# Optimization experiments

Measured on AMD Instinct MI355X. Metric: run time of the kernel, lower is better.

Reference implementation:

```python
import jax, jax.numpy as jnp
import numpy as np

D_MODEL = 1024
NUM_HEADS = 16
D_FF = 4096
NEG_INF = -1e9


def _linear_params(key, d_in, d_out):
    kw, kb = jax.random.split(key)
    bound = 1.0 / np.sqrt(d_in)
    W = jax.random.uniform(kw, (d_in, d_out), jnp.float32, -bound, bound)
    b = jax.random.uniform(kb, (d_out,), jnp.float32, -bound, bound)
    return W, b


def setup_inputs() -> dict:
    key = jax.random.key(0)
    ks = jax.random.split(key, 8)
    B, S = 2, 2048
    x = jax.random.normal(ks[0], (B, S, D_MODEL), jnp.float32)
    # causal mask: 1 = attend, 0 = masked
    mask = jnp.tril(jnp.ones((S, S), jnp.bool_))[None, :, :]
    Wq, bq = _linear_params(ks[1], D_MODEL, D_MODEL)
    Wk, bk = _linear_params(ks[2], D_MODEL, D_MODEL)
    Wv, bv = _linear_params(ks[3], D_MODEL, D_MODEL)
    Wo, bo = _linear_params(ks[4], D_MODEL, D_MODEL)
    W1, b1 = _linear_params(ks[5], D_MODEL, D_FF)
    W2, b2 = _linear_params(ks[6], D_FF, D_MODEL)
    ln1_g = jnp.ones((D_MODEL,), jnp.float32)
    ln1_b = jnp.zeros((D_MODEL,), jnp.float32)
    ln2_g = jnp.ones((D_MODEL,), jnp.float32)
    ln2_b = jnp.zeros((D_MODEL,), jnp.float32)
    return {"x": x, "mask": mask,
            "Wq": Wq, "bq": bq, "Wk": Wk, "bk": bk, "Wv": Wv, "bv": bv,
            "Wo": Wo, "bo": bo, "W1": W1, "b1": b1, "W2": W2, "b2": b2,
            "ln1_g": ln1_g, "ln1_b": ln1_b, "ln2_g": ln2_g, "ln2_b": ln2_b}


def layer_norm(x, g, b, eps=1e-5):
    mu = jnp.mean(x, axis=-1, keepdims=True)
    var = jnp.mean(jnp.square(x - mu), axis=-1, keepdims=True)
    return (x - mu) * jax.lax.rsqrt(var + eps) * g + b


def attention(xn, mask, Wq, bq, Wk, bk, Wv, bv, Wo, bo):
    B, S, D = xn.shape
    H, dk = NUM_HEADS, D // NUM_HEADS
    q = (xn @ Wq + bq).reshape(B, S, H, dk).transpose(0, 2, 1, 3)  # [B,H,S,dk]
    k = (xn @ Wk + bk).reshape(B, S, H, dk).transpose(0, 2, 1, 3)
    v = (xn @ Wv + bv).reshape(B, S, H, dk).transpose(0, 2, 1, 3)
    scores = jnp.einsum("bhsd,bhtd->bhst", q, k) / jnp.sqrt(jnp.float32(dk))
    scores = jnp.where(mask[:, None, :, :], scores, NEG_INF)
    attn = jax.nn.softmax(scores, axis=-1)
    out = jnp.einsum("bhst,bhtd->bhsd", attn, v)  # [B,H,S,dk]
    out = out.transpose(0, 2, 1, 3).reshape(B, S, D)
    return out @ Wo + bo


def reference(x, mask, Wq, bq, Wk, bk, Wv, bv, Wo, bo, W1, b1, W2, b2,
              ln1_g, ln1_b, ln2_g, ln2_b):
    # pre-norm MHA + residual (dropout = identity at eval)
    h = x + attention(layer_norm(x, ln1_g, ln1_b), mask,
                      Wq, bq, Wk, bk, Wv, bv, Wo, bo)
    # pre-norm FFN + residual
    ff = jax.nn.relu(layer_norm(h, ln2_g, ln2_b) @ W1 + b1) @ W2 + b2
    return h + ff
```

## Files before the change

### kernel.cpp

```cpp
#include <hip/hip_runtime.h>

typedef unsigned short u16;
typedef __attribute__((ext_vector_type(8))) short    s16x8;
typedef __attribute__((ext_vector_type(8))) unsigned short u16x8;
typedef __attribute__((ext_vector_type(4))) float    f32x4;

typedef __attribute__((address_space(1))) const void gvoid_c;
typedef __attribute__((address_space(3))) void       lvoid;

__device__ __forceinline__ float b2f(u16 x) {
    return __builtin_bit_cast(float, (unsigned)x << 16);
}
__device__ __forceinline__ u16 f2bf(float f) {
    unsigned u = __builtin_bit_cast(unsigned, f);
    return (u16)((u + 0x7FFFu + ((u >> 16) & 1u)) >> 16);
}
__device__ __forceinline__ void gld16(const void* g, void* l) {
    __builtin_amdgcn_global_load_lds((gvoid_c*)g, (lvoid*)l, 16, 0, 0);
}

__global__ __launch_bounds__(256) void transpose_f2b(
    const float* __restrict__ in, u16* __restrict__ out, int R, int C)
{
    __shared__ u16 tile[32][33];
    int tx = threadIdx.x & 31, ty = threadIdx.x >> 5;
    int c0 = blockIdx.x * 32, r0 = blockIdx.y * 32;
#pragma unroll
    for (int i = 0; i < 32; i += 8)
        tile[ty + i][tx] = f2bf(in[(size_t)(r0 + ty + i) * C + c0 + tx]);
    __syncthreads();
#pragma unroll
    for (int i = 0; i < 32; i += 8)
        out[(size_t)(c0 + ty + i) * R + r0 + tx] = tile[tx][ty + i];
}

__global__ void concat3(const float* a, const float* b, const float* c, float* o) {
    int i = blockIdx.x * blockDim.x + threadIdx.x;
    o[i] = (i < 1024) ? a[i] : (i < 2048 ? b[i - 1024] : c[i - 2048]);
}

__global__ __launch_bounds__(256) void ln_k(
    const float* __restrict__ in, const float* __restrict__ gg,
    const float* __restrict__ bb, u16* __restrict__ out)
{
    const int D = 1024;
    int row  = blockIdx.x * 4 + (threadIdx.x >> 6);
    int lane = threadIdx.x & 63;
    const float* ip = in + (size_t)row * D;
    float v[16];
#pragma unroll
    for (int cc = 0; cc < 4; cc++) {
        f32x4 t = *(const f32x4*)(ip + cc * 256 + lane * 4);
#pragma unroll
        for (int i = 0; i < 4; i++) v[cc * 4 + i] = t[i];
    }
    float s1 = 0.f, s2 = 0.f;
#pragma unroll
    for (int i = 0; i < 16; i++) { s1 += v[i]; s2 += v[i] * v[i]; }
#pragma unroll
    for (int m = 1; m < 64; m <<= 1) { s1 += __shfl_xor(s1, m); s2 += __shfl_xor(s2, m); }
    float mu   = s1 * (1.f / 1024.f);
    float var  = s2 * (1.f / 1024.f) - mu * mu;
    float rstd = rsqrtf(var + 1e-5f);
#pragma unroll
    for (int cc = 0; cc < 4; cc++) {
        int e = cc * 256 + lane * 4;
        f32x4 gv = *(const f32x4*)(gg + e);
        f32x4 bv = *(const f32x4*)(bb + e);
        u16 o[4];
#pragma unroll
        for (int i = 0; i < 4; i++)
            o[i] = f2bf((v[cc * 4 + i] - mu) * rstd * gv[i] + bv[i]);
        *(__attribute__((ext_vector_type(4))) unsigned short*)(out + (size_t)row * D + e) =
            (__attribute__((ext_vector_type(4))) unsigned short){o[0], o[1], o[2], o[3]};
    }
}

template <int RES, bool RELU, bool OUTF32>
__global__ __launch_bounds__(256) void gemm_bt(
    const u16* __restrict__ A, const u16* __restrict__ Bt,
    const float* __restrict__ bias, const float* __restrict__ res,
    void* __restrict__ out, int M, int N, int K)
{
    __shared__ u16 As[4096];
    __shared__ u16 Bs[4096];
    int tid = threadIdx.x, wave = tid >> 6, lane = tid & 63;
    int g = lane >> 4, c = lane & 15;
    int wm = wave >> 1, wn = wave & 1;
    int m0 = blockIdx.y * 128, n0 = blockIdx.x * 128;

    f32x4 acc[4][4];
#pragma unroll
    for (int m = 0; m < 4; m++)
#pragma unroll
        for (int n = 0; n < 4; n++) acc[m][n] = (f32x4){0, 0, 0, 0};

    int ch0 = wave * 128 + lane, ch1 = ch0 + 64;
    const u16* Ag0 = A  + (size_t)(m0 + (ch0 >> 2)) * K + (ch0 & 3) * 8;
    const u16* Ag1 = A  + (size_t)(m0 + (ch1 >> 2)) * K + (ch1 & 3) * 8;
    const u16* Bg0 = Bt + (size_t)(n0 + (ch0 >> 2)) * K + (ch0 & 3) * 8;
    const u16* Bg1 = Bt + (size_t)(n0 + (ch1 >> 2)) * K + (ch1 & 3) * 8;
    u16* Al0 = &As[wave * 1024];
    u16* Al1 = &As[wave * 1024 + 512];
    u16* Bl0 = &Bs[wave * 1024];
    u16* Bl1 = &Bs[wave * 1024 + 512];

    for (int k0 = 0; k0 < K; k0 += 32) {
        __syncthreads();
        gld16(Ag0, Al0); gld16(Ag1, Al1);
        gld16(Bg0, Bl0); gld16(Bg1, Bl1);
        Ag0 += 32; Ag1 += 32; Bg0 += 32; Bg1 += 32;
        __syncthreads();
        s16x8 af[4], bfr[4];
#pragma unroll
        for (int m = 0; m < 4; m++)
            af[m] = *(const s16x8*)&As[(wm * 64 + m * 16 + c) * 32 + g * 8];
#pragma unroll
        for (int n = 0; n < 4; n++)
            bfr[n] = *(const s16x8*)&Bs[(wn * 64 + n * 16 + c) * 32 + g * 8];
#pragma unroll
        for (int m = 0; m < 4; m++)
#pragma unroll
            for (int n = 0; n < 4; n++)
                acc[m][n] = __builtin_amdgcn_mfma_f32_16x16x32_bf16(af[m], bfr[n], acc[m][n], 0, 0, 0);
    }

#pragma unroll
    for (int n = 0; n < 4; n++) {
        int col = n0 + wn * 64 + n * 16 + c;
        float bb = bias[col];
#pragma unroll
        for (int m = 0; m < 4; m++) {
#pragma unroll
            for (int j = 0; j < 4; j++) {
                int row = m0 + wm * 64 + m * 16 + g * 4 + j;
                float v = acc[m][n][j] + bb;
                if (RES == 2) v += res[(size_t)row * N + col];
                if (RELU) v = fmaxf(v, 0.f);
                if (OUTF32) ((float*)out)[(size_t)row * N + col] = v;
                else        ((u16*)out)[(size_t)row * N + col] = f2bf(v);
            }
        }
    }
}

template <int RES, bool RELU, bool OUTF32>
__global__ __launch_bounds__(256) void gemm_bt_n64(
    const u16* __restrict__ A, const u16* __restrict__ Bt,
    const float* __restrict__ bias, const float* __restrict__ res,
    void* __restrict__ out, int M, int N, int K)
{
    __shared__ u16 As[4096];
    __shared__ u16 Bs[2048];
    int tid = threadIdx.x, wave = tid >> 6, lane = tid & 63;
    int g = lane >> 4, c = lane & 15;
    int wm = wave >> 1, wn = wave & 1;
    int m0 = blockIdx.y * 128, n0 = blockIdx.x * 64;

    f32x4 acc[4][2];
#pragma unroll
    for (int m = 0; m < 4; m++)
#pragma unroll
        for (int n = 0; n < 2; n++) acc[m][n] = (f32x4){0, 0, 0, 0};

    int ch0 = wave * 128 + lane, ch1 = ch0 + 64;
    int chb = wave * 64 + lane;
    const u16* Ag0 = A  + (size_t)(m0 + (ch0 >> 2)) * K + (ch0 & 3) * 8;
    const u16* Ag1 = A  + (size_t)(m0 + (ch1 >> 2)) * K + (ch1 & 3) * 8;
    const u16* Bg0 = Bt + (size_t)(n0 + (chb >> 2)) * K + (chb & 3) * 8;
    u16* Al0 = &As[wave * 1024];
    u16* Al1 = &As[wave * 1024 + 512];
    u16* Bl0 = &Bs[wave * 512];

    for (int k0 = 0; k0 < K; k0 += 32) {
        __syncthreads();
        gld16(Ag0, Al0); gld16(Ag1, Al1);
        gld16(Bg0, Bl0);
        Ag0 += 32; Ag1 += 32; Bg0 += 32;
        __syncthreads();
        s16x8 af[4], bfr[2];
#pragma unroll
        for (int m = 0; m < 4; m++)
            af[m] = *(const s16x8*)&As[(wm * 64 + m * 16 + c) * 32 + g * 8];
#pragma unroll
        for (int n = 0; n < 2; n++)
            bfr[n] = *(const s16x8*)&Bs[(wn * 32 + n * 16 + c) * 32 + g * 8];
#pragma unroll
        for (int m = 0; m < 4; m++)
#pragma unroll
            for (int n = 0; n < 2; n++)
                acc[m][n] = __builtin_amdgcn_mfma_f32_16x16x32_bf16(af[m], bfr[n], acc[m][n], 0, 0, 0);
    }

#pragma unroll
    for (int n = 0; n < 2; n++) {
        int col = n0 + wn * 32 + n * 16 + c;
        float bb = bias[col];
#pragma unroll
        for (int m = 0; m < 4; m++) {
#pragma unroll
            for (int j = 0; j < 4; j++) {
                int row = m0 + wm * 64 + m * 16 + g * 4 + j;
                float v = acc[m][n][j] + bb;
                if (RES == 2) v += res[(size_t)row * N + col];
                if (RELU) v = fmaxf(v, 0.f);
                if (OUTF32) ((float*)out)[(size_t)row * N + col] = v;
                else        ((u16*)out)[(size_t)row * N + col] = f2bf(v);
            }
        }
    }
}

__global__ __launch_bounds__(256) void v_transpose(
    const u16* __restrict__ qkv, u16* __restrict__ vt)
{
    const int S = 2048, NC = 3072;
    __shared__ u16 tile[64][72];
    int st = blockIdx.x, bh = blockIdx.y, b = bh >> 4, h = bh & 15;
    int tid = threadIdx.x;
    int i = tid >> 3, cb8 = (tid & 7) * 8;
    const u16* src = qkv + (size_t)(b * S + st * 64) * NC + 2048 + h * 64;
    u16x8 a0 = *(const u16x8*)(src + (size_t)i * NC + cb8);
    u16x8 a1 = *(const u16x8*)(src + (size_t)(i + 32) * NC + cb8);
    *(u16x8*)&tile[i][cb8]      = a0;
    *(u16x8*)&tile[i + 32][cb8] = a1;
    __syncthreads();
    int d = tid >> 3, e8 = (tid & 7) * 8;
    int m = (d & 7) * 8;
#pragma unroll
    for (int rr = 0; rr < 2; rr++) {
        int r = d + rr * 32;
        u16x8 o;
#pragma unroll
        for (int j = 0; j < 8; j++) o[j] = tile[(e8 ^ m) + j][r];
        *(u16x8*)(vt + ((size_t)bh * 64 + r) * 2048 + st * 64 + e8) = o;
    }
}

__global__ __launch_bounds__(256) void attn_fwd2(
    const u16* __restrict__ qkv, const u16* __restrict__ vt,
    u16* __restrict__ o)
{
    const int S = 2048, NC = 3072;
    __shared__ u16 Ks[4096];
    __shared__ u16 Vs[4096];
    __shared__ u16 Plds[4][16][72];
    int qp = blockIdx.x, bh = blockIdx.y, b = bh >> 4, h = bh & 15;
    int tid = threadIdx.x, wave = tid >> 6, lane = tid & 63;
    int g = lane >> 4, c = lane & 15;
    int sr = tid >> 3, scb8 = (tid & 7) * 8;
    int mS = (sr & 7) * 8;
    int mR = (c & 7) * 8;

    const u16* kbase = qkv + (size_t)b * S * NC + 1024 + h * 64;
    const u16* vbase = vt + (size_t)bh * 64 * 2048;

#pragma unroll 1
    for (int ph = 0; ph < 2; ph++) {
        int qt = ph ? qp : 31 - qp;
        int q0 = qt * 64 + wave * 16;
        const u16* qptr = qkv + (size_t)(b * S + q0 + c) * NC + h * 64;
        s16x8 qf0 = *(const s16x8*)(qptr + g * 8);
        s16x8 qf1 = *(const s16x8*)(qptr + 32 + g * 8);

        float mr[4], lr[4];
        f32x4 acc[4];
#pragma unroll
        for (int j = 0; j < 4; j++) { mr[j] = -1e30f; lr[j] = 0.f; }
#pragma unroll
        for (int n = 0; n < 4; n++) acc[n] = (f32x4){0, 0, 0, 0};

        int ntiles = qt + 1;
        for (int t = 0; t < ntiles; t++) {
            int t0 = t * 64;
            __syncthreads();
            gld16(kbase + (size_t)(t0 + sr)      * NC + (scb8 ^ mS), &Ks[wave * 512]);
            gld16(kbase + (size_t)(t0 + sr + 32) * NC + (scb8 ^ mS), &Ks[2048 + wave * 512]);
            gld16(vbase + (size_t)sr        * 2048 + t0 + scb8, &Vs[wave * 512]);
            gld16(vbase + (size_t)(sr + 32) * 2048 + t0 + scb8, &Vs[2048 + wave * 512]);
            __syncthreads();

            f32x4 s[4];
#pragma unroll
            for (int kt = 0; kt < 4; kt++) {
                int r = kt * 16 + c;
                s16x8 kf0 = *(const s16x8*)&Ks[r * 64 + ((g * 8) ^ mR)];
                s16x8 kf1 = *(const s16x8*)&Ks[r * 64 + ((32 + g * 8) ^ mR)];
                f32x4 sv = (f32x4){0, 0, 0, 0};
                sv = __builtin_amdgcn_mfma_f32_16x16x32_bf16(qf0, kf0, sv, 0, 0, 0);
                sv = __builtin_amdgcn_mfma_f32_16x16x32_bf16(qf1, kf1, sv, 0, 0, 0);
                s[kt] = sv;
            }
#pragma unroll
            for (int kt = 0; kt < 4; kt++) {
                int kcol = t0 + kt * 16 + c;
#pragma unroll
                for (int j = 0; j < 4; j++) {
                    int qrow = q0 + g * 4 + j;
                    s[kt][j] = (kcol <= qrow) ? s[kt][j] * 0.125f : -1e30f;
                }
            }
#pragma unroll
            for (int j = 0; j < 4; j++) {
                float tm = fmaxf(fmaxf(s[0][j], s[1][j]), fmaxf(s[2][j], s[3][j]));
#pragma unroll
                for (int m = 1; m < 16; m <<= 1) tm = fmaxf(tm, __shfl_xor(tm, m));
                float mnew = fmaxf(mr[j], tm);
                float corr = __expf(mr[j] - mnew);
                float rs = 0.f;
#pragma unroll
                for (int kt = 0; kt < 4; kt++) { float p = __expf(s[kt][j] - mnew); s[kt][j] = p; rs += p; }
#pragma unroll
                for (int m = 1; m < 16; m <<= 1) rs += __shfl_xor(rs, m);
                lr[j] = lr[j] * corr + rs;
                mr[j] = mnew;
#pragma unroll
                for (int n = 0; n < 4; n++) acc[n][j] *= corr;
            }
#pragma unroll
            for (int kt = 0; kt < 4; kt++)
#pragma unroll
                for (int j = 0; j < 4; j++)
                    Plds[wave][g * 4 + j][kt * 16 + c] = f2bf(s[kt][j]);
            s16x8 pa0 = *(const s16x8*)&Plds[wave][c][g * 8];
            s16x8 pa1 = *(const s16x8*)&Plds[wave][c][32 + g * 8];
#pragma unroll
            for (int n = 0; n < 4; n++) {
                int r = n * 16 + c;
                s16x8 vb0 = *(const s16x8*)&Vs[r * 64 + ((g * 8) ^ mR)];
                s16x8 vb1 = *(const s16x8*)&Vs[r * 64 + ((32 + g * 8) ^ mR)];
                acc[n] = __builtin_amdgcn_mfma_f32_16x16x32_bf16(pa0, vb0, acc[n], 0, 0, 0);
                acc[n] = __builtin_amdgcn_mfma_f32_16x16x32_bf16(pa1, vb1, acc[n], 0, 0, 0);
            }
        }
#pragma unroll
        for (int j = 0; j < 4; j++) {
            float inv = 1.f / lr[j];
            size_t rbase = (size_t)(b * S + q0 + g * 4 + j) * 1024 + h * 64;
#pragma unroll
            for (int n = 0; n < 4; n++)
                o[rbase + n * 16 + c] = f2bf(acc[n][j] * inv);
        }
    }
}

extern "C" void kernel_launch(void* const* d_in, const int* in_sizes, int n_in,
                              void* d_out, int out_size, void* d_ws, size_t ws_size,
                              hipStream_t stream)
{
    const float* x    = (const float*)d_in[0];
    const float* Wq   = (const float*)d_in[2];  const float* bq = (const float*)d_in[3];
    const float* Wk   = (const float*)d_in[4];  const float* bk = (const float*)d_in[5];
    const float* Wv   = (const float*)d_in[6];  const float* bv = (const float*)d_in[7];
    const float* Wo   = (const float*)d_in[8];  const float* bo = (const float*)d_in[9];
    const float* W1   = (const float*)d_in[10]; const float* b1 = (const float*)d_in[11];
    const float* W2   = (const float*)d_in[12]; const float* b2 = (const float*)d_in[13];
    const float* ln1g = (const float*)d_in[14]; const float* ln1b = (const float*)d_in[15];
    const float* ln2g = (const float*)d_in[16]; const float* ln2b = (const float*)d_in[17];

    unsigned char* ws = (unsigned char*)d_ws;
    u16*   Wqkv_t = (u16*)(ws + 0);
    u16*   Wo_t   = (u16*)(ws + 6291456);
    u16*   W1_t   = (u16*)(ws + 8388608);
    u16*   W2_t   = (u16*)(ws + 16777216);
    float* bqkv   = (float*)(ws + 25165824);
    u16*   lnbuf  = (u16*)(ws + 25178112);
    u16*   qkvbuf = (u16*)(ws + 33566720);
    u16*   attnb  = (u16*)(ws + 58732544);
    u16*   f1buf  = (u16*)(ws + 33566720);
    float* hbuf   = (float*)(ws + 67121152);
    u16*   vtbuf  = (u16*)(ws + 67121152);

    transpose_f2b<<<dim3(32, 32), 256, 0, stream>>>(Wq, Wqkv_t,               1024, 1024);
    transpose_f2b<<<dim3(32, 32), 256, 0, stream>>>(Wk, Wqkv_t + 1024 * 1024, 1024, 1024);
    transpose_f2b<<<dim3(32, 32), 256, 0, stream>>>(Wv, Wqkv_t + 2048 * 1024, 1024, 1024);
    transpose_f2b<<<dim3(32, 32), 256, 0, stream>>>(Wo, Wo_t,                 1024, 1024);
    transpose_f2b<<<dim3(128, 32), 256, 0, stream>>>(W1, W1_t,                1024, 4096);
    transpose_f2b<<<dim3(32, 128), 256, 0, stream>>>(W2, W2_t,                4096, 1024);
    concat3<<<12, 256, 0, stream>>>(bq, bk, bv, bqkv);

    ln_k<<<1024, 256, 0, stream>>>(x, ln1g, ln1b, lnbuf);
    gemm_bt<0, false, false><<<dim3(24, 32), 256, 0, stream>>>(
        lnbuf, Wqkv_t, bqkv, nullptr, qkvbuf, 4096, 3072, 1024);
    v_transpose<<<dim3(32, 32), 256, 0, stream>>>(qkvbuf, vtbuf);
    attn_fwd2<<<dim3(16, 32), 256, 0, stream>>>(qkvbuf, vtbuf, attnb);

    gemm_bt_n64<2, false, true><<<dim3(16, 32), 256, 0, stream>>>(
        attnb, Wo_t, bo, x, hbuf, 4096, 1024, 1024);

    ln_k<<<1024, 256, 0, stream>>>(hbuf, ln2g, ln2b, lnbuf);
    gemm_bt<0, true, false><<<dim3(32, 32), 256, 0, stream>>>(
        lnbuf, W1_t, b1, nullptr, f1buf, 4096, 4096, 1024);
    gemm_bt_n64<2, false, true><<<dim3(16, 32), 256, 0, stream>>>(
        f1buf, W2_t, b2, hbuf, (float*)d_out, 4096, 1024, 4096);
}
```

Baseline: 431.4 us.

## Double-buffer GEMM LDS staging and split-K the FFN2 GEMM with atomics

Merges the two GEMM kernels into one templated kernel that double-buffers the LDS tiles, so the next K-slice's global-to-LDS load is issued while the current slice runs MFMAs, and one barrier per iteration is dropped. The FFN down-projection (K=4096) now uses 128-wide tiles with a 4-way split-K over blockIdx.z. A separate init kernel writes residual plus bias into the output first, and the partial sums are then accumulated with relaxed fp32 atomics. This aims to hide load latency and improve occupancy for the long-K GEMM, at the cost of doubled LDS per block, atomic traffic, and summation order that can vary from run to run.

After: 445.3 us. 1.03x slower.

```diff
diff --git a/kernel.cpp b/kernel.cpp
--- a/kernel.cpp
+++ b/kernel.cpp
@@ -76,136 +76,103 @@
     }
 }
 
-template <int RES, bool RELU, bool OUTF32>
-__global__ __launch_bounds__(256) void gemm_bt(
+__global__ __launch_bounds__(256) void ffn2_init(
+    const float* __restrict__ h, const float* __restrict__ b2,
+    float* __restrict__ out)
+{
+    int i = blockIdx.x * 256 + threadIdx.x;
+    f32x4 hv = ((const f32x4*)h)[i];
+    f32x4 bv = ((const f32x4*)b2)[i & 255];
+    ((f32x4*)out)[i] = hv + bv;
+}
+
+template <int BN, int RES, bool RELU, bool OUTF32, bool ATOMIC>
+__global__ __launch_bounds__(256) void gemm2(
     const u16* __restrict__ A, const u16* __restrict__ Bt,
     const float* __restrict__ bias, const float* __restrict__ res,
-    void* __restrict__ out, int M, int N, int K)
-{
-    __shared__ u16 As[4096];
-    __shared__ u16 Bs[4096];
+    void* __restrict__ out, int M, int N, int K, int KC)
+{
+    constexpr int NFR = BN / 32;
+    __shared__ u16 As[2][4096];
+    __shared__ u16 Bs[2][BN * 32];
     int tid = threadIdx.x, wave = tid >> 6, lane = tid & 63;
     int g = lane >> 4, c = lane & 15;
     int wm = wave >> 1, wn = wave & 1;
-    int m0 = blockIdx.y * 128, n0 = blockIdx.x * 128;
-
-    f32x4 acc[4][4];
+    int m0 = blockIdx.y * 128, n0 = blockIdx.x * BN;
+    int kst = blockIdx.z * KC;
+
+    f32x4 acc[4][NFR];
 #pragma unroll
     for (int m = 0; m < 4; m++)
 #pragma unroll
-        for (int n = 0; n < 4; n++) acc[m][n] = (f32x4){0, 0, 0, 0};
+        for (int n = 0; n < NFR; n++) acc[m][n] = (f32x4){0, 0, 0, 0};
 
     int ch0 = wave * 128 + lane, ch1 = ch0 + 64;
-    const u16* Ag0 = A  + (size_t)(m0 + (ch0 >> 2)) * K + (ch0 & 3) * 8;
-    const u16* Ag1 = A  + (size_t)(m0 + (ch1 >> 2)) * K + (ch1 & 3) * 8;
-    const u16* Bg0 = Bt + (size_t)(n0 + (ch0 >> 2)) * K + (ch0 & 3) * 8;
-    const u16* Bg1 = Bt + (size_t)(n0 + (ch1 >> 2)) * K + (ch1 & 3) * 8;
-    u16* Al0 = &As[wave * 1024];
-    u16* Al1 = &As[wave * 1024 + 512];
-    u16* Bl0 = &Bs[wave * 1024];
-    u16* Bl1 = &Bs[wave * 1024 + 512];
-
-    for (int k0 = 0; k0 < K; k0 += 32) {
+    const u16* Ag0 = A + (size_t)(m0 + (ch0 >> 2)) * K + kst + (ch0 & 3) * 8;
+    const u16* Ag1 = A + (size_t)(m0 + (ch1 >> 2)) * K + kst + (ch1 & 3) * 8;
+    const u16* Bg0;
+    const u16* Bg1 = nullptr;
+    if constexpr (BN == 128) {
+        Bg0 = Bt + (size_t)(n0 + (ch0 >> 2)) * K + kst + (ch0 & 3) * 8;
+        Bg1 = Bt + (size_t)(n0 + (ch1 >> 2)) * K + kst + (ch1 & 3) * 8;
+    } else {
+        int chb = wave * 64 + lane;
+        Bg0 = Bt + (size_t)(n0 + (chb >> 2)) * K + kst + (chb & 3) * 8;
+    }
+
+    auto stage = [&](int buf, int kk) {
+        gld16(Ag0 + kk, &As[buf][wave * 1024]);
+        gld16(Ag1 + kk, &As[buf][wave * 1024 + 512]);
+        if constexpr (BN == 128) {
+            gld16(Bg0 + kk, &Bs[buf][wave * 1024]);
+            gld16(Bg1 + kk, &Bs[buf][wave * 1024 + 512]);
+        } else {
+            gld16(Bg0 + kk, &Bs[buf][wave * 512]);
+        }
+    };
+
+    int nt = KC / 32;
+    stage(0, 0);
+    __syncthreads();
+    int cur = 0;
+    for (int t = 0; t < nt; t++) {
+        if (t + 1 < nt) stage(cur ^ 1, (t + 1) * 32);
+        s16x8 af[4], bfr[NFR];
+#pragma unroll
+        for (int m = 0; m < 4; m++)
+            af[m] = *(const s16x8*)&As[cur][(wm * 64 + m * 16 + c) * 32 + g * 8];
+#pragma unroll
+        for (int n = 0; n < NFR; n++)
+            bfr[n] = *(const s16x8*)&Bs[cur][(wn * (BN / 2) + n * 16 + c) * 32 + g * 8];
+#pragma unroll
+        for (int m = 0; m < 4; m++)
+#pragma unroll
+            for (int n = 0; n < NFR; n++)
+                acc[m][n] = __builtin_amdgcn_mfma_f32_16x16x32_bf16(af[m], bfr[n], acc[m][n], 0, 0, 0);
         __syncthreads();
-        gld16(Ag0, Al0); gld16(Ag1, Al1);
-        gld16(Bg0, Bl0); gld16(Bg1, Bl1);
-        Ag0 += 32; Ag1 += 32; Bg0 += 32; Bg1 += 32;
-        __syncthreads();
-        s16x8 af[4], bfr[4];
-#pragma unroll
-        for (int m = 0; m < 4; m++)
-            af[m] = *(const s16x8*)&As[(wm * 64 + m * 16 + c) * 32 + g * 8];
-#pragma unroll
-        for (int n = 0; n < 4; n++)
-            bfr[n] = *(const s16x8*)&Bs[(wn * 64 + n * 16 + c) * 32 + g * 8];
-#pragma unroll
-        for (int m = 0; m < 4; m++)
-#pragma unroll
-            for (int n = 0; n < 4; n++)
-                acc[m][n] = __builtin_amdgcn_mfma_f32_16x16x32_bf16(af[m], bfr[n], acc[m][n], 0, 0, 0);
-    }
-
-#pragma unroll
-    for (int n = 0; n < 4; n++) {
-        int col = n0 + wn * 64 + n * 16 + c;
-        float bb = bias[col];
+        cur ^= 1;
+    }
+
+#pragma unroll
+    for (int n = 0; n < NFR; n++) {
+        int col = n0 + wn * (BN / 2) + n * 16 + c;
+        float bb = 0.f;
+        if constexpr (!ATOMIC) bb = bias[col];
 #pragma unroll
         for (int m = 0; m < 4; m++) {
 #pragma unroll
             for (int j = 0; j < 4; j++) {
                 int row = m0 + wm * 64 + m * 16 + g * 4 + j;
                 float v = acc[m][n][j] + bb;
-                if (RES == 2) v += res[(size_t)row * N + col];
-                if (RELU) v = fmaxf(v, 0.f);
-                if (OUTF32) ((float*)out)[(size_t)row * N + col] = v;
-                else        ((u16*)out)[(size_t)row * N + col] = f2bf(v);
-            }
-        }
-    }
-}
-
-template <int RES, bool RELU, bool OUTF32>
-__global__ __launch_bounds__(256) void gemm_bt_n64(
-    const u16* __restrict__ A, const u16* __restrict__ Bt,
-    const float* __restrict__ bias, const float* __restrict__ res,
-    void* __restrict__ out, int M, int N, int K)
-{
-    __shared__ u16 As[4096];
-    __shared__ u16 Bs[2048];
-    int tid = threadIdx.x, wave = tid >> 6, lane = tid & 63;
-    int g = lane >> 4, c = lane & 15;
-    int wm = wave >> 1, wn = wave & 1;
-    int m0 = blockIdx.y * 128, n0 = blockIdx.x * 64;
-
-    f32x4 acc[4][2];
-#pragma unroll
-    for (int m = 0; m < 4; m++)
-#pragma unroll
-        for (int n = 0; n < 2; n++) acc[m][n] = (f32x4){0, 0, 0, 0};
-
-    int ch0 = wave * 128 + lane, ch1 = ch0 + 64;
-    int chb = wave * 64 + lane;
-    const u16* Ag0 = A  + (size_t)(m0 + (ch0 >> 2)) * K + (ch0 & 3) * 8;
-    const u16* Ag1 = A  + (size_t)(m0 + (ch1 >> 2)) * K + (ch1 & 3) * 8;
-    const u16* Bg0 = Bt + (size_t)(n0 + (chb >> 2)) * K + (chb & 3) * 8;
-    u16* Al0 = &As[wave * 1024];
-    u16* Al1 = &As[wave * 1024 + 512];
-    u16* Bl0 = &Bs[wave * 512];
-
-    for (int k0 = 0; k0 < K; k0 += 32) {
-        __syncthreads();
-        gld16(Ag0, Al0); gld16(Ag1, Al1);
-        gld16(Bg0, Bl0);
-        Ag0 += 32; Ag1 += 32; Bg0 += 32;
-        __syncthreads();
-        s16x8 af[4], bfr[2];
-#pragma unroll
-        for (int m = 0; m < 4; m++)
-            af[m] = *(const s16x8*)&As[(wm * 64 + m * 16 + c) * 32 + g * 8];
-#pragma unroll
-        for (int n = 0; n < 2; n++)
-            bfr[n] = *(const s16x8*)&Bs[(wn * 32 + n * 16 + c) * 32 + g * 8];
-#pragma unroll
-        for (int m = 0; m < 4; m++)
-#pragma unroll
-            for (int n = 0; n < 2; n++)
-                acc[m][n] = __builtin_amdgcn_mfma_f32_16x16x32_bf16(af[m], bfr[n], acc[m][n], 0, 0, 0);
-    }
-
-#pragma unroll
-    for (int n = 0; n < 2; n++) {
-        int col = n0 + wn * 32 + n * 16 + c;
-        float bb = bias[col];
-#pragma unroll
-        for (int m = 0; m < 4; m++) {
-#pragma unroll
-            for (int j = 0; j < 4; j++) {
-                int row = m0 + wm * 64 + m * 16 + g * 4 + j;
-                float v = acc[m][n][j] + bb;
-                if (RES == 2) v += res[(size_t)row * N + col];
-                if (RELU) v = fmaxf(v, 0.f);
-                if (OUTF32) ((float*)out)[(size_t)row * N + col] = v;
-                else        ((u16*)out)[(size_t)row * N + col] = f2bf(v);
+                if constexpr (RES == 2) v += res[(size_t)row * N + col];
+                if constexpr (RELU) v = fmaxf(v, 0.f);
+                if constexpr (ATOMIC)
+                    __hip_atomic_fetch_add(&((float*)out)[(size_t)row * N + col], v,
+                                           __ATOMIC_RELAXED, __HIP_MEMORY_SCOPE_AGENT);
+                else if constexpr (OUTF32)
+                    ((float*)out)[(size_t)row * N + col] = v;
+                else
+                    ((u16*)out)[(size_t)row * N + col] = f2bf(v);
             }
         }
     }
@@ -380,17 +347,18 @@
     concat3<<<12, 256, 0, stream>>>(bq, bk, bv, bqkv);
 
     ln_k<<<1024, 256, 0, stream>>>(x, ln1g, ln1b, lnbuf);
-    gemm_bt<0, false, false><<<dim3(24, 32), 256, 0, stream>>>(
-        lnbuf, Wqkv_t, bqkv, nullptr, qkvbuf, 4096, 3072, 1024);
+    gemm2<128, 0, false, false, false><<<dim3(24, 32, 1), 256, 0, stream>>>(
+        lnbuf, Wqkv_t, bqkv, nullptr, qkvbuf, 4096, 3072, 1024, 1024);
     v_transpose<<<dim3(32, 32), 256, 0, stream>>>(qkvbuf, vtbuf);
     attn_fwd2<<<dim3(16, 32), 256, 0, stream>>>(qkvbuf, vtbuf, attnb);
 
-    gemm_bt_n64<2, false, true><<<dim3(16, 32), 256, 0, stream>>>(
-        attnb, Wo_t, bo, x, hbuf, 4096, 1024, 1024);
+    gemm2<64, 2, false, true, false><<<dim3(16, 32, 1), 256, 0, stream>>>(
+        attnb, Wo_t, bo, x, hbuf, 4096, 1024, 1024, 1024);
 
     ln_k<<<1024, 256, 0, stream>>>(hbuf, ln2g, ln2b, lnbuf);
-    gemm_bt<0, true, false><<<dim3(32, 32), 256, 0, stream>>>(
-        lnbuf, W1_t, b1, nullptr, f1buf, 4096, 4096, 1024);
-    gemm_bt_n64<2, false, true><<<dim3(16, 32), 256, 0, stream>>>(
-        f1buf, W2_t, b2, hbuf, (float*)d_out, 4096, 1024, 4096);
-}
+    gemm2<128, 0, true, false, false><<<dim3(32, 32, 1), 256, 0, stream>>>(
+        lnbuf, W1_t, b1, nullptr, f1buf, 4096, 4096, 1024, 1024);
+    ffn2_init<<<4096, 256, 0, stream>>>(hbuf, b2, (float*)d_out);
+    gemm2<128, 0, false, true, true><<<dim3(8, 32, 4), 256, 0, stream>>>(
+        f1buf, W2_t, b2, nullptr, d_out, 4096, 1024, 4096, 1024);
+}
```
